# Optimization experiments

Hardware: AMD Instinct MI355X
Metric: run time of the kernel (lower is better)

## Reference

```python
import jax, jax.numpy as jnp
import numpy as np

HEADS = 8
DIM_HEAD = 64
QUERY_DIM = 512
CONTEXT_DIM = 768
INNER = HEADS * DIM_HEAD  # 512
SCALE = DIM_HEAD ** -0.5


def setup_inputs() -> dict:
    key = jax.random.key(0)
    ks = jax.random.split(key, 7)
    B, N, M = 4, 2048, 2048
    x = jax.random.normal(ks[0], (B, N, QUERY_DIM), dtype=jnp.float32)
    context = jax.random.normal(ks[1], (B, M, CONTEXT_DIM), dtype=jnp.float32)
    # torch Linear weights: [out_features, in_features], y = x @ W.T
    s = 0.02
    Wq = jax.random.normal(ks[2], (INNER, QUERY_DIM), dtype=jnp.float32) * s
    Wk = jax.random.normal(ks[3], (INNER, CONTEXT_DIM), dtype=jnp.float32) * s
    Wv = jax.random.normal(ks[4], (INNER, CONTEXT_DIM), dtype=jnp.float32) * s
    Wo = jax.random.normal(ks[5], (QUERY_DIM, INNER), dtype=jnp.float32) * s
    bo = jax.random.normal(ks[6], (QUERY_DIM,), dtype=jnp.float32) * s
    return {"x": x, "context": context, "Wq": Wq, "Wk": Wk, "Wv": Wv, "Wo": Wo, "bo": bo}


def reference(x, context, Wq, Wk, Wv, Wo, bo):
    b, n, _ = x.shape
    m = context.shape[1]
    h, d = HEADS, DIM_HEAD
    # Projections (bias=False for q/k/v)
    q = jnp.einsum('bnc,ec->bne', x, Wq)        # [b, n, inner]
    k = jnp.einsum('bmc,ec->bme', context, Wk)  # [b, m, inner]
    v = jnp.einsum('bmc,ec->bme', context, Wv)
    # Split heads
    q = q.reshape(b, n, h, d)
    k = k.reshape(b, m, h, d)
    v = v.reshape(b, m, h, d)
    # Scores in fp32 (original casts q,k to float), scaled by dim_head**-0.5
    sim = jnp.einsum('bihd,bjhd->bhij', q.astype(jnp.float32), k.astype(jnp.float32)) * SCALE
    attn = jax.nn.softmax(sim, axis=-1).astype(v.dtype)
    out = jnp.einsum('bhij,bjhd->bihd', attn, v).reshape(b, n, h * d)
    # Output projection with bias (dropout=0 -> identity)
    return jnp.einsum('bne,oe->bno', out, Wo) + bo
```

## Files before the change

### kernel.cpp

```cpp
#include <hip/hip_runtime.h>
#include <hip/hip_bf16.h>
#include <math.h>


typedef __bf16 bf16x8 __attribute__((ext_vector_type(8)));
typedef __bf16 bf16x4 __attribute__((ext_vector_type(4)));
typedef short s16x4 __attribute__((ext_vector_type(4)));
typedef float f32x4 __attribute__((ext_vector_type(4)));

#define QSCALE 0.18033688011112042f

#if __has_builtin(__builtin_amdgcn_exp2f)
#define EXP2(x) __builtin_amdgcn_exp2f(x)
#else
#define EXP2(x) exp2f(x)
#endif

__device__ __forceinline__ f32x4 mfma32(bf16x8 a, bf16x8 b, f32x4 c) {
  return __builtin_amdgcn_mfma_f32_16x16x32_bf16(a, b, c, 0, 0, 0);
}
__device__ __forceinline__ f32x4 mfma16(s16x4 a, s16x4 b, f32x4 c) {
  return __builtin_amdgcn_mfma_f32_16x16x16bf16_1k(a, b, c, 0, 0, 0);
}

__device__ __forceinline__ void glds16(const void* g, void* l) {
  __builtin_amdgcn_global_load_lds(
      (const __attribute__((address_space(1))) unsigned int*)g,
      (__attribute__((address_space(3))) unsigned int*)l, 16, 0, 0);
}

__global__ __launch_bounds__(256) void cast_all(
    const float* __restrict__ x, const float* __restrict__ ctx,
    const float* __restrict__ wq, const float* __restrict__ wk,
    const float* __restrict__ wv, const float* __restrict__ wo,
    __bf16* __restrict__ xb, __bf16* __restrict__ cb,
    __bf16* __restrict__ wqb, __bf16* __restrict__ wkb,
    __bf16* __restrict__ wvb, __bf16* __restrict__ wob) {
  const int B0 = 1048576;
  const int B1 = 2621440;
  const int B2 = 2686976;
  const int B3 = 2785280;
  const int B4 = 2883584;
  const int B5 = 2949120;
  for (int i = blockIdx.x * blockDim.x + threadIdx.x; i < B5;
       i += gridDim.x * blockDim.x) {
    const float* s;
    __bf16* d;
    int off;
    if (i < B0)      { s = x;   d = xb;  off = i; }
    else if (i < B1) { s = ctx; d = cb;  off = i - B0; }
    else if (i < B2) { s = wq;  d = wqb; off = i - B1; }
    else if (i < B3) { s = wk;  d = wkb; off = i - B2; }
    else if (i < B4) { s = wv;  d = wvb; off = i - B3; }
    else             { s = wo;  d = wob; off = i - B4; }
    float4 f = ((const float4*)s)[off];
    union { __bf16 b[4]; ushort4 u; } cv;
    cv.b[0] = (__bf16)f.x; cv.b[1] = (__bf16)f.y;
    cv.b[2] = (__bf16)f.z; cv.b[3] = (__bf16)f.w;
    ((ushort4*)d)[off] = cv.u;
  }
}

template <int MODE>
__device__ __forceinline__ void gemm_body(
    const __bf16* __restrict__ A, const __bf16* __restrict__ B,
    __bf16* __restrict__ Cout, int Kd, float scale, int m0, int n0,
    __bf16 (*As)[4][128][8], __bf16 (*Bs)[4][128][8]) {
  const int t = threadIdx.x;
  const int w = t >> 6;
  const int lane = t & 63;
  const int ln = lane & 15;
  const int qd = lane >> 4;
  const int wm = (w >> 1) * 64;
  const int wn = (w & 1) * 64;

  f32x4 zero4 = {0.f, 0.f, 0.f, 0.f};
  f32x4 acc[4][4];
#pragma unroll
  for (int i = 0; i < 4; ++i)
#pragma unroll
    for (int j = 0; j < 4; ++j) acc[i][j] = zero4;

  const __bf16* gA0 = A + (size_t)(m0 + lane) * Kd + w * 8;
  const __bf16* gA1 = A + (size_t)(m0 + 64 + lane) * Kd + w * 8;
  const __bf16* gB0 = B + (size_t)(n0 + lane) * Kd + w * 8;
  const __bf16* gB1 = B + (size_t)(n0 + 64 + lane) * Kd + w * 8;

  glds16(gA0, &As[0][w][0][0]);
  glds16(gA1, &As[0][w][64][0]);
  glds16(gB0, &Bs[0][w][0][0]);
  glds16(gB1, &Bs[0][w][64][0]);

  int buf = 0;
  for (int kc = 0; kc < Kd; kc += 32) {
    __syncthreads();
    if (kc + 32 < Kd) {
      glds16(gA0 + kc + 32, &As[buf ^ 1][w][0][0]);
      glds16(gA1 + kc + 32, &As[buf ^ 1][w][64][0]);
      glds16(gB0 + kc + 32, &Bs[buf ^ 1][w][0][0]);
      glds16(gB1 + kc + 32, &Bs[buf ^ 1][w][64][0]);
    }
    bf16x8 af[4], bfr[4];
#pragma unroll
    for (int i = 0; i < 4; ++i) {
      af[i] = *(const bf16x8*)&As[buf][qd][wm + i * 16 + ln][0];
      bfr[i] = *(const bf16x8*)&Bs[buf][qd][wn + i * 16 + ln][0];
    }
#pragma unroll
    for (int i = 0; i < 4; ++i)
#pragma unroll
      for (int j = 0; j < 4; ++j) {
        if (MODE == 1)
          acc[i][j] = mfma32(af[i], bfr[j], acc[i][j]);
        else
          acc[i][j] = mfma32(bfr[j], af[i], acc[i][j]);
      }
    buf ^= 1;
  }

#pragma unroll
  for (int i = 0; i < 4; ++i)
#pragma unroll
    for (int j = 0; j < 4; ++j) {
      if (MODE == 0) {
        const int gm = m0 + wm + i * 16 + ln;
        const int gn0 = n0 + wn + j * 16 + qd * 4;
        const int bb = gm >> 11, tok = gm & 2047;
        const int hh = gn0 >> 6, dd0 = gn0 & 63;
        bf16x4 v;
#pragma unroll
        for (int rg = 0; rg < 4; ++rg) v[rg] = (__bf16)(acc[i][j][rg] * scale);
        *(bf16x4*)(Cout + (((size_t)bb * 8 + hh) * 2048 + tok) * 64 + dd0) = v;
      } else {
        const int gm0 = m0 + wm + i * 16 + qd * 4;
        const int gn = n0 + wn + j * 16 + ln;
        const int bb = gm0 >> 11, tok0 = gm0 & 2047;
        const int hh = gn >> 6, dd = gn & 63;
        bf16x4 v;
#pragma unroll
        for (int rg = 0; rg < 4; ++rg) v[rg] = (__bf16)acc[i][j][rg];
        *(bf16x4*)(Cout + (((size_t)bb * 8 + hh) * 64 + dd) * 2048 + tok0) = v;
      }
    }
}

__global__ __launch_bounds__(256, 3) void proj_qkv(
    const __bf16* __restrict__ xb, const __bf16* __restrict__ cb,
    const __bf16* __restrict__ Wq, const __bf16* __restrict__ Wk,
    const __bf16* __restrict__ Wv, __bf16* __restrict__ Qw,
    __bf16* __restrict__ Kw, __bf16* __restrict__ Vtw) {
  __shared__ __align__(16) __bf16 As[2][4][128][8];
  __shared__ __align__(16) __bf16 Bs[2][4][128][8];
  const int m0 = blockIdx.x * 128;
  const int job = blockIdx.y >> 2;
  const int n0 = (blockIdx.y & 3) * 128;
  if (job == 0)
    gemm_body<0>(xb, Wq, Qw, 512, QSCALE, m0, n0, As, Bs);
  else if (job == 1)
    gemm_body<0>(cb, Wk, Kw, 768, 1.0f, m0, n0, As, Bs);
  else
    gemm_body<1>(cb, Wv, Vtw, 768, 1.0f, m0, n0, As, Bs);
}

__global__ __launch_bounds__(256) void gemm_out(
    const __bf16* __restrict__ O0, const __bf16* __restrict__ O1,
    const float* __restrict__ lbuf,
    const __bf16* __restrict__ B,
    float* __restrict__ C, const float* __restrict__ bias) {
  const int m0 = blockIdx.x * 64;
  const int n0 = blockIdx.y * 128;
  const int t = threadIdx.x;
  const int w = t >> 6;
  const int lane = t & 63;
  const int ln = lane & 15;
  const int qd = lane >> 4;
  const int wm = (w >> 1) * 32;
  const int wn = (w & 1) * 64;

  __shared__ __align__(16) __bf16 As[2][64][40];
  __shared__ __align__(16) __bf16 Bs[2][4][128][8];

  f32x4 zero4 = {0.f, 0.f, 0.f, 0.f};
  f32x4 acc[2][4];
#pragma unroll
  for (int i = 0; i < 2; ++i)
#pragma unroll
    for (int j = 0; j < 4; ++j) acc[i][j] = zero4;

  const int ra = t >> 2, ca = (t & 3) * 8;
  const int gm_s = m0 + ra;
  const int bidx = gm_s >> 11, tok_s = gm_s & 2047;
  const size_t aoff = (size_t)gm_s * 512 + ca;
  const __bf16* gB0 = B + (size_t)(n0 + lane) * 512 + w * 8;
  const __bf16* gB1 = B + (size_t)(n0 + 64 + lane) * 512 + w * 8;

  float inv[8];
#pragma unroll
  for (int hh = 0; hh < 8; ++hh) {
    const float l0 = lbuf[((size_t)bidx * 8 + hh) * 2048 + tok_s];
    const float l1 = lbuf[65536 + ((size_t)bidx * 8 + hh) * 2048 + tok_s];
    inv[hh] = 1.0f / (l0 + l1);
  }

  {
    union { bf16x8 v; uint4 u; } u0, u1, rr;
    u0.u = *(const uint4*)(O0 + aoff);
    u1.u = *(const uint4*)(O1 + aoff);
    glds16(gB0, &Bs[0][w][0][0]);
    glds16(gB1, &Bs[0][w][64][0]);
    const float iv = inv[0];
#pragma unroll
    for (int e = 0; e < 8; ++e)
      rr.v[e] = (__bf16)(((float)u0.v[e] + (float)u1.v[e]) * iv);
    *(uint4*)&As[0][ra][ca] = rr.u;
  }

  int buf = 0;
#pragma unroll
  for (int k = 0; k < 16; ++k) {
    __syncthreads();
    uint4 o0n, o1n;
    if (k < 15) {
      o0n = *(const uint4*)(O0 + aoff + (k + 1) * 32);
      o1n = *(const uint4*)(O1 + aoff + (k + 1) * 32);
      glds16(gB0 + (k + 1) * 32, &Bs[buf ^ 1][w][0][0]);
      glds16(gB1 + (k + 1) * 32, &Bs[buf ^ 1][w][64][0]);
    }
    bf16x8 af[2], bfr[4];
#pragma unroll
    for (int i = 0; i < 2; ++i)
      af[i] = *(const bf16x8*)&As[buf][wm + i * 16 + ln][qd * 8];
#pragma unroll
    for (int j = 0; j < 4; ++j)
      bfr[j] = *(const bf16x8*)&Bs[buf][qd][wn + j * 16 + ln][0];
#pragma unroll
    for (int i = 0; i < 2; ++i)
#pragma unroll
      for (int j = 0; j < 4; ++j)
        acc[i][j] = mfma32(bfr[j], af[i], acc[i][j]);
    if (k < 15) {
      union { bf16x8 v; uint4 u; } u0, u1, rr;
      u0.u = o0n;
      u1.u = o1n;
      const float iv = inv[(k + 1) >> 1];
#pragma unroll
      for (int e = 0; e < 8; ++e)
        rr.v[e] = (__bf16)(((float)u0.v[e] + (float)u1.v[e]) * iv);
      *(uint4*)&As[buf ^ 1][ra][ca] = rr.u;
    }
    buf ^= 1;
  }

#pragma unroll
  for (int i = 0; i < 2; ++i)
#pragma unroll
    for (int j = 0; j < 4; ++j) {
      const int gm = m0 + wm + i * 16 + ln;
      const int gn0 = n0 + wn + j * 16 + qd * 4;
      f32x4 bi = *(const f32x4*)&bias[gn0];
      f32x4 v = acc[i][j] + bi;
      *(f32x4*)&C[(size_t)gm * 512 + gn0] = v;
    }
}

__global__ __launch_bounds__(256, 4) void attn_kernel(
    const __bf16* __restrict__ Q,
    const __bf16* __restrict__ K,
    const __bf16* __restrict__ Vt,
    __bf16* __restrict__ Oh,
    float* __restrict__ lbuf) {
  const int S = 2048;
  const int qt = blockIdx.x;
  const int bh = blockIdx.y;
  const int sp = blockIdx.z;
  const int b = bh >> 3, h = bh & 7;
  const int t = threadIdx.x;
  const int w = t >> 6;
  const int lane = t & 63;
  const int ln = lane & 15;
  const int qd = lane >> 4;

  __shared__ __align__(16) __bf16 Ks[128][72];
  __shared__ __align__(16) __bf16 Vts[64][132];

  bf16x8 bq[2][2];
  {
    const __bf16* qb =
        Q + ((size_t)bh * S + qt * 128 + w * 32 + ln) * 64 + qd * 8;
#pragma unroll
    for (int mt = 0; mt < 2; ++mt)
#pragma unroll
      for (int kst = 0; kst < 2; ++kst)
        bq[mt][kst] = *(const bf16x8*)(qb + mt * 1024 + kst * 32);
  }

  f32x4 zero4 = {0.f, 0.f, 0.f, 0.f};
  f32x4 o[2][4];
  f32x4 o_l[2];
#pragma unroll
  for (int mt = 0; mt < 2; ++mt) {
#pragma unroll
    for (int i = 0; i < 4; ++i) o[mt][i] = zero4;
    o_l[mt] = zero4;
  }
  const s16x4 ones = {0x3F80, 0x3F80, 0x3F80, 0x3F80};

  const int kr = t >> 1, kc = (t & 1) * 32;
  const int vd = t >> 2, vc = (t & 3) * 32;
  const int kt0 = sp * 8;

  for (int kt = kt0; kt < kt0 + 8; ++kt) {
    const uint4* gK =
        (const uint4*)(K + ((size_t)bh * S + kt * 128 + kr) * 64 + kc);
    const uint4* gV =
        (const uint4*)(Vt + ((size_t)bh * 64 + vd) * S + kt * 128 + vc);
    uint4 kv0 = gK[0], kv1 = gK[1], kv2 = gK[2], kv3 = gK[3];
    uint4 vv0 = gV[0], vv1 = gV[1], vv2 = gV[2], vv3 = gV[3];
    __syncthreads();
    {
      uint4* dK = (uint4*)&Ks[kr][kc];
      dK[0] = kv0; dK[1] = kv1; dK[2] = kv2; dK[3] = kv3;
      uint2* dV = (uint2*)&Vts[vd][vc];
      dV[0] = *(uint2*)&vv0; dV[1] = *((uint2*)&vv0 + 1);
      dV[2] = *(uint2*)&vv1; dV[3] = *((uint2*)&vv1 + 1);
      dV[4] = *(uint2*)&vv2; dV[5] = *((uint2*)&vv2 + 1);
      dV[6] = *(uint2*)&vv3; dV[7] = *((uint2*)&vv3 + 1);
    }
    __syncthreads();

#pragma unroll
    for (int c = 0; c < 4; ++c) {
      f32x4 s[2][2];
      s[0][0] = zero4; s[0][1] = zero4; s[1][0] = zero4; s[1][1] = zero4;
#pragma unroll
      for (int e = 0; e < 2; ++e) {
        const int nt = c * 2 + e;
#pragma unroll
        for (int kst = 0; kst < 2; ++kst) {
          bf16x8 ak = *(const bf16x8*)&Ks[nt * 16 + ln][kst * 32 + qd * 8];
          s[e][0] = mfma32(ak, bq[0][kst], s[e][0]);
          s[e][1] = mfma32(ak, bq[1][kst], s[e][1]);
        }
      }
#pragma unroll
      for (int e = 0; e < 2; ++e)
#pragma unroll
        for (int mt = 0; mt < 2; ++mt)
#pragma unroll
          for (int rg = 0; rg < 4; ++rg) s[e][mt][rg] = EXP2(s[e][mt][rg]);
#pragma unroll
      for (int e = 0; e < 2; ++e) {
        const int nt = c * 2 + e;
        bf16x4 c0, c1;
#pragma unroll
        for (int rg = 0; rg < 4; ++rg) {
          c0[rg] = (__bf16)s[e][0][rg];
          c1[rg] = (__bf16)s[e][1][rg];
        }
        s16x4 p0 = __builtin_bit_cast(s16x4, c0);
        s16x4 p1 = __builtin_bit_cast(s16x4, c1);
        o_l[0] = mfma16(ones, p0, o_l[0]);
        o_l[1] = mfma16(ones, p1, o_l[1]);
#pragma unroll
        for (int i = 0; i < 4; ++i) {
          bf16x4 av = *(const bf16x4*)&Vts[i * 16 + ln][nt * 16 + qd * 4];
          s16x4 a = __builtin_bit_cast(s16x4, av);
          o[0][i] = mfma16(a, p0, o[0][i]);
          o[1][i] = mfma16(a, p1, o[1][i]);
        }
      }
    }
  }

  __bf16* Osp = Oh + (size_t)sp * 8192 * 512;
#pragma unroll
  for (int mt = 0; mt < 2; ++mt) {
    const int tok = qt * 128 + w * 32 + mt * 16 + ln;
    if (qd == 0) lbuf[((size_t)sp * 32 + bh) * 2048 + tok] = o_l[mt][0];
#pragma unroll
    for (int i = 0; i < 4; ++i) {
      bf16x4 v;
#pragma unroll
      for (int rg = 0; rg < 4; ++rg) v[rg] = (__bf16)o[mt][i][rg];
      const int col = h * 64 + i * 16 + qd * 4;
      *(bf16x4*)&Osp[((size_t)b * S + tok) * 512 + col] = v;
    }
  }
}

extern "C" void kernel_launch(void* const* d_in, const int* in_sizes, int n_in,
                              void* d_out, int out_size, void* d_ws,
                              size_t ws_size, hipStream_t stream) {
  const float* x = (const float*)d_in[0];
  const float* ctx = (const float*)d_in[1];
  const float* Wq = (const float*)d_in[2];
  const float* Wk = (const float*)d_in[3];
  const float* Wv = (const float*)d_in[4];
  const float* Wo = (const float*)d_in[5];
  const float* bo = (const float*)d_in[6];

  char* p = (char*)d_ws;
  __bf16* xb = (__bf16*)p;   p += (size_t)8192 * 512 * 2;
  __bf16* cb = (__bf16*)p;   p += (size_t)8192 * 768 * 2;
  __bf16* wqb = (__bf16*)p;  p += (size_t)512 * 512 * 2;
  __bf16* wkb = (__bf16*)p;  p += (size_t)512 * 768 * 2;
  __bf16* wvb = (__bf16*)p;  p += (size_t)512 * 768 * 2;
  __bf16* wob = (__bf16*)p;  p += (size_t)512 * 512 * 2;
  __bf16* Qw = (__bf16*)p;   p += (size_t)8192 * 512 * 2;
  __bf16* Kw = (__bf16*)p;   p += (size_t)8192 * 512 * 2;
  __bf16* Vtw = (__bf16*)p;  p += (size_t)8192 * 512 * 2;
  __bf16* Oh = (__bf16*)p;   p += (size_t)2 * 8192 * 512 * 2;
  float* lbuf = (float*)p;   p += (size_t)2 * 32 * 2048 * 4;

  cast_all<<<2880, 256, 0, stream>>>(x, ctx, Wq, Wk, Wv, Wo, xb, cb, wqb, wkb,
                                     wvb, wob);

  dim3 gp(64, 12);
  proj_qkv<<<gp, 256, 0, stream>>>(xb, cb, wqb, wkb, wvb, Qw, Kw, Vtw);

  dim3 ga(16, 32, 2);
  attn_kernel<<<ga, 256, 0, stream>>>(Qw, Kw, Vtw, Oh, lbuf);

  dim3 go(128, 4);
  gemm_out<<<go, 256, 0, stream>>>(Oh, Oh + (size_t)8192 * 512, lbuf, wob,
                                   (float*)d_out, bo);
}
```

Measured before the change: 204.0 us.

## Use 16x16x32 MFMA for PV and replace async LDS loads with register staging

The attention PV product and row-sum now use the 16x16x32 bf16 MFMA instead of pairs of 16x16x16 ops. K rows are stored in LDS under a permuted row order and V is held in a chunked layout, so each lane's 8-element P fragment lines up with one bf16x8 V read. Both projection GEMMs drop global_load_lds double buffering in favour of register-prefetched 64-wide K tiles in padded single-buffer LDS. The PV change halves the number of MFMA issues for that step. The GEMM change trades async copies and double buffering for register staging, which adds registers and an extra barrier per tile.

```diff
diff --git a/kernel.cpp b/kernel.cpp
--- a/kernel.cpp
+++ b/kernel.cpp
@@ -5,7 +5,6 @@
 
 typedef __bf16 bf16x8 __attribute__((ext_vector_type(8)));
 typedef __bf16 bf16x4 __attribute__((ext_vector_type(4)));
-typedef short s16x4 __attribute__((ext_vector_type(4)));
 typedef float f32x4 __attribute__((ext_vector_type(4)));
 
 #define QSCALE 0.18033688011112042f
@@ -18,15 +17,6 @@
 
 __device__ __forceinline__ f32x4 mfma32(bf16x8 a, bf16x8 b, f32x4 c) {
   return __builtin_amdgcn_mfma_f32_16x16x32_bf16(a, b, c, 0, 0, 0);
-}
-__device__ __forceinline__ f32x4 mfma16(s16x4 a, s16x4 b, f32x4 c) {
-  return __builtin_amdgcn_mfma_f32_16x16x16bf16_1k(a, b, c, 0, 0, 0);
-}
-
-__device__ __forceinline__ void glds16(const void* g, void* l) {
-  __builtin_amdgcn_global_load_lds(
-      (const __attribute__((address_space(1))) unsigned int*)g,
-      (__attribute__((address_space(3))) unsigned int*)l, 16, 0, 0);
 }
 
 __global__ __launch_bounds__(256) void cast_all(
@@ -63,9 +53,9 @@
 
 template <int MODE>
 __device__ __forceinline__ void gemm_body(
-    const __bf16* __restrict__ A, const __bf16* __restrict__ B,
+    const __bf16* __restrict__ A, const __bf16* __restrict__ W,
     __bf16* __restrict__ Cout, int Kd, float scale, int m0, int n0,
-    __bf16 (*As)[4][128][8], __bf16 (*Bs)[4][128][8]) {
+    __bf16 (*As)[72], __bf16 (*Bs)[72]) {
   const int t = threadIdx.x;
   const int w = t >> 6;
   const int lane = t & 63;
@@ -81,41 +71,53 @@
 #pragma unroll
     for (int j = 0; j < 4; ++j) acc[i][j] = zero4;
 
-  const __bf16* gA0 = A + (size_t)(m0 + lane) * Kd + w * 8;
-  const __bf16* gA1 = A + (size_t)(m0 + 64 + lane) * Kd + w * 8;
-  const __bf16* gB0 = B + (size_t)(n0 + lane) * Kd + w * 8;
-  const __bf16* gB1 = B + (size_t)(n0 + 64 + lane) * Kd + w * 8;
-
-  glds16(gA0, &As[0][w][0][0]);
-  glds16(gA1, &As[0][w][64][0]);
-  glds16(gB0, &Bs[0][w][0][0]);
-  glds16(gB1, &Bs[0][w][64][0]);
-
-  int buf = 0;
-  for (int kc = 0; kc < Kd; kc += 32) {
-    __syncthreads();
-    if (kc + 32 < Kd) {
-      glds16(gA0 + kc + 32, &As[buf ^ 1][w][0][0]);
-      glds16(gA1 + kc + 32, &As[buf ^ 1][w][64][0]);
-      glds16(gB0 + kc + 32, &Bs[buf ^ 1][w][0][0]);
-      glds16(gB1 + kc + 32, &Bs[buf ^ 1][w][64][0]);
-    }
-    bf16x8 af[4], bfr[4];
-#pragma unroll
-    for (int i = 0; i < 4; ++i) {
-      af[i] = *(const bf16x8*)&As[buf][qd][wm + i * 16 + ln][0];
-      bfr[i] = *(const bf16x8*)&Bs[buf][qd][wn + i * 16 + ln][0];
-    }
-#pragma unroll
-    for (int i = 0; i < 4; ++i)
-#pragma unroll
-      for (int j = 0; j < 4; ++j) {
-        if (MODE == 1)
-          acc[i][j] = mfma32(af[i], bfr[j], acc[i][j]);
-        else
-          acc[i][j] = mfma32(bfr[j], af[i], acc[i][j]);
+  const int r0 = t >> 2;
+  const int c0 = (t & 3) * 16;
+  const __bf16* gA0 = A + (size_t)(m0 + r0) * Kd + c0;
+  const __bf16* gA1 = A + (size_t)(m0 + r0 + 64) * Kd + c0;
+  const __bf16* gB0 = W + (size_t)(n0 + r0) * Kd + c0;
+  const __bf16* gB1 = W + (size_t)(n0 + r0 + 64) * Kd + c0;
+
+  uint4 a00 = *(const uint4*)gA0, a01 = *(const uint4*)(gA0 + 8);
+  uint4 a10 = *(const uint4*)gA1, a11 = *(const uint4*)(gA1 + 8);
+  uint4 b00 = *(const uint4*)gB0, b01 = *(const uint4*)(gB0 + 8);
+  uint4 b10 = *(const uint4*)gB1, b11 = *(const uint4*)(gB1 + 8);
+
+  for (int kc = 0; kc < Kd; kc += 64) {
+    __syncthreads();
+    *(uint4*)&As[r0][c0] = a00;       *(uint4*)&As[r0][c0 + 8] = a01;
+    *(uint4*)&As[r0 + 64][c0] = a10;  *(uint4*)&As[r0 + 64][c0 + 8] = a11;
+    *(uint4*)&Bs[r0][c0] = b00;       *(uint4*)&Bs[r0][c0 + 8] = b01;
+    *(uint4*)&Bs[r0 + 64][c0] = b10;  *(uint4*)&Bs[r0 + 64][c0 + 8] = b11;
+    __syncthreads();
+    if (kc + 64 < Kd) {
+      a00 = *(const uint4*)(gA0 + kc + 64);
+      a01 = *(const uint4*)(gA0 + kc + 72);
+      a10 = *(const uint4*)(gA1 + kc + 64);
+      a11 = *(const uint4*)(gA1 + kc + 72);
+      b00 = *(const uint4*)(gB0 + kc + 64);
+      b01 = *(const uint4*)(gB0 + kc + 72);
+      b10 = *(const uint4*)(gB1 + kc + 64);
+      b11 = *(const uint4*)(gB1 + kc + 72);
+    }
+#pragma unroll
+    for (int kst = 0; kst < 2; ++kst) {
+      bf16x8 af[4], bfr[4];
+#pragma unroll
+      for (int i = 0; i < 4; ++i) {
+        af[i] = *(const bf16x8*)&As[wm + i * 16 + ln][kst * 32 + qd * 8];
+        bfr[i] = *(const bf16x8*)&Bs[wn + i * 16 + ln][kst * 32 + qd * 8];
       }
-    buf ^= 1;
+#pragma unroll
+      for (int i = 0; i < 4; ++i)
+#pragma unroll
+        for (int j = 0; j < 4; ++j) {
+          if (MODE == 1)
+            acc[i][j] = mfma32(af[i], bfr[j], acc[i][j]);
+          else
+            acc[i][j] = mfma32(bfr[j], af[i], acc[i][j]);
+        }
+    }
   }
 
 #pragma unroll
@@ -149,8 +151,8 @@
     const __bf16* __restrict__ Wq, const __bf16* __restrict__ Wk,
     const __bf16* __restrict__ Wv, __bf16* __restrict__ Qw,
     __bf16* __restrict__ Kw, __bf16* __restrict__ Vtw) {
-  __shared__ __align__(16) __bf16 As[2][4][128][8];
-  __shared__ __align__(16) __bf16 Bs[2][4][128][8];
+  __shared__ __align__(16) __bf16 As[128][72];
+  __shared__ __align__(16) __bf16 Bs[128][72];
   const int m0 = blockIdx.x * 128;
   const int job = blockIdx.y >> 2;
   const int n0 = (blockIdx.y & 3) * 128;
@@ -177,8 +179,8 @@
   const int wm = (w >> 1) * 32;
   const int wn = (w & 1) * 64;
 
-  __shared__ __align__(16) __bf16 As[2][64][40];
-  __shared__ __align__(16) __bf16 Bs[2][4][128][8];
+  __shared__ __align__(16) __bf16 As[64][72];
+  __shared__ __align__(16) __bf16 Bs[128][72];
 
   f32x4 zero4 = {0.f, 0.f, 0.f, 0.f};
   f32x4 acc[2][4];
@@ -187,12 +189,13 @@
 #pragma unroll
     for (int j = 0; j < 4; ++j) acc[i][j] = zero4;
 
-  const int ra = t >> 2, ca = (t & 3) * 8;
-  const int gm_s = m0 + ra;
+  const int r0 = t >> 2;
+  const int c0 = (t & 3) * 16;
+  const int gm_s = m0 + r0;
   const int bidx = gm_s >> 11, tok_s = gm_s & 2047;
-  const size_t aoff = (size_t)gm_s * 512 + ca;
-  const __bf16* gB0 = B + (size_t)(n0 + lane) * 512 + w * 8;
-  const __bf16* gB1 = B + (size_t)(n0 + 64 + lane) * 512 + w * 8;
+  const size_t aoff = (size_t)gm_s * 512 + c0;
+  const __bf16* gB0 = B + (size_t)(n0 + r0) * 512 + c0;
+  const __bf16* gB1 = B + (size_t)(n0 + r0 + 64) * 512 + c0;
 
   float inv[8];
 #pragma unroll
@@ -202,53 +205,53 @@
     inv[hh] = 1.0f / (l0 + l1);
   }
 
-  {
-    union { bf16x8 v; uint4 u; } u0, u1, rr;
-    u0.u = *(const uint4*)(O0 + aoff);
-    u1.u = *(const uint4*)(O1 + aoff);
-    glds16(gB0, &Bs[0][w][0][0]);
-    glds16(gB1, &Bs[0][w][64][0]);
-    const float iv = inv[0];
+  uint4 o00 = *(const uint4*)(O0 + aoff), o01 = *(const uint4*)(O0 + aoff + 8);
+  uint4 o10 = *(const uint4*)(O1 + aoff), o11 = *(const uint4*)(O1 + aoff + 8);
+  uint4 b00 = *(const uint4*)gB0, b01 = *(const uint4*)(gB0 + 8);
+  uint4 b10 = *(const uint4*)gB1, b11 = *(const uint4*)(gB1 + 8);
+
+  for (int kc = 0; kc < 512; kc += 64) {
+    const float iv = inv[kc >> 6];
+    union { bf16x8 v; uint4 u; } u0, u1, r0v, r1v;
+    u0.u = o00; u1.u = o10;
 #pragma unroll
     for (int e = 0; e < 8; ++e)
-      rr.v[e] = (__bf16)(((float)u0.v[e] + (float)u1.v[e]) * iv);
-    *(uint4*)&As[0][ra][ca] = rr.u;
-  }
-
-  int buf = 0;
-#pragma unroll
-  for (int k = 0; k < 16; ++k) {
-    __syncthreads();
-    uint4 o0n, o1n;
-    if (k < 15) {
-      o0n = *(const uint4*)(O0 + aoff + (k + 1) * 32);
-      o1n = *(const uint4*)(O1 + aoff + (k + 1) * 32);
-      glds16(gB0 + (k + 1) * 32, &Bs[buf ^ 1][w][0][0]);
-      glds16(gB1 + (k + 1) * 32, &Bs[buf ^ 1][w][64][0]);
-    }
-    bf16x8 af[2], bfr[4];
-#pragma unroll
-    for (int i = 0; i < 2; ++i)
-      af[i] = *(const bf16x8*)&As[buf][wm + i * 16 + ln][qd * 8];
-#pragma unroll
-    for (int j = 0; j < 4; ++j)
-      bfr[j] = *(const bf16x8*)&Bs[buf][qd][wn + j * 16 + ln][0];
-#pragma unroll
-    for (int i = 0; i < 2; ++i)
+      r0v.v[e] = (__bf16)(((float)u0.v[e] + (float)u1.v[e]) * iv);
+    u0.u = o01; u1.u = o11;
+#pragma unroll
+    for (int e = 0; e < 8; ++e)
+      r1v.v[e] = (__bf16)(((float)u0.v[e] + (float)u1.v[e]) * iv);
+    __syncthreads();
+    *(uint4*)&As[r0][c0] = r0v.u;
+    *(uint4*)&As[r0][c0 + 8] = r1v.u;
+    *(uint4*)&Bs[r0][c0] = b00;       *(uint4*)&Bs[r0][c0 + 8] = b01;
+    *(uint4*)&Bs[r0 + 64][c0] = b10;  *(uint4*)&Bs[r0 + 64][c0 + 8] = b11;
+    __syncthreads();
+    if (kc + 64 < 512) {
+      o00 = *(const uint4*)(O0 + aoff + kc + 64);
+      o01 = *(const uint4*)(O0 + aoff + kc + 72);
+      o10 = *(const uint4*)(O1 + aoff + kc + 64);
+      o11 = *(const uint4*)(O1 + aoff + kc + 72);
+      b00 = *(const uint4*)(gB0 + kc + 64);
+      b01 = *(const uint4*)(gB0 + kc + 72);
+      b10 = *(const uint4*)(gB1 + kc + 64);
+      b11 = *(const uint4*)(gB1 + kc + 72);
+    }
+#pragma unroll
+    for (int kst = 0; kst < 2; ++kst) {
+      bf16x8 af[2], bfr[4];
+#pragma unroll
+      for (int i = 0; i < 2; ++i)
+        af[i] = *(const bf16x8*)&As[wm + i * 16 + ln][kst * 32 + qd * 8];
 #pragma unroll
       for (int j = 0; j < 4; ++j)
-        acc[i][j] = mfma32(bfr[j], af[i], acc[i][j]);
-    if (k < 15) {
-      union { bf16x8 v; uint4 u; } u0, u1, rr;
-      u0.u = o0n;
-      u1.u = o1n;
-      const float iv = inv[(k + 1) >> 1];
-#pragma unroll
-      for (int e = 0; e < 8; ++e)
-        rr.v[e] = (__bf16)(((float)u0.v[e] + (float)u1.v[e]) * iv);
-      *(uint4*)&As[buf ^ 1][ra][ca] = rr.u;
-    }
-    buf ^= 1;
+        bfr[j] = *(const bf16x8*)&Bs[wn + j * 16 + ln][kst * 32 + qd * 8];
+#pragma unroll
+      for (int i = 0; i < 2; ++i)
+#pragma unroll
+        for (int j = 0; j < 4; ++j)
+          acc[i][j] = mfma32(bfr[j], af[i], acc[i][j]);
+    }
   }
 
 #pragma unroll
@@ -281,7 +284,7 @@
   const int qd = lane >> 4;
 
   __shared__ __align__(16) __bf16 Ks[128][72];
-  __shared__ __align__(16) __bf16 Vts[64][132];
+  __shared__ __align__(16) __bf16 V4[4][64][40];
 
   bf16x8 bq[2][2];
   {
@@ -303,28 +306,33 @@
     for (int i = 0; i < 4; ++i) o[mt][i] = zero4;
     o_l[mt] = zero4;
   }
-  const s16x4 ones = {0x3F80, 0x3F80, 0x3F80, 0x3F80};
+  bf16x8 ones8;
+  {
+    union { unsigned short u[8]; bf16x8 v; } U;
+#pragma unroll
+    for (int e = 0; e < 8; ++e) U.u[e] = 0x3F80;
+    ones8 = U.v;
+  }
 
   const int kr = t >> 1, kc = (t & 1) * 32;
-  const int vd = t >> 2, vc = (t & 3) * 32;
+  const int krow =
+      (kr & ~31) | ((kr & 4) << 2) | (((kr >> 3) & 3) << 2) | (kr & 3);
+  const int vd = t >> 2, cV = t & 3;
   const int kt0 = sp * 8;
 
   for (int kt = kt0; kt < kt0 + 8; ++kt) {
     const uint4* gK =
         (const uint4*)(K + ((size_t)bh * S + kt * 128 + kr) * 64 + kc);
     const uint4* gV =
-        (const uint4*)(Vt + ((size_t)bh * 64 + vd) * S + kt * 128 + vc);
+        (const uint4*)(Vt + ((size_t)bh * 64 + vd) * S + kt * 128 + cV * 32);
     uint4 kv0 = gK[0], kv1 = gK[1], kv2 = gK[2], kv3 = gK[3];
     uint4 vv0 = gV[0], vv1 = gV[1], vv2 = gV[2], vv3 = gV[3];
     __syncthreads();
     {
-      uint4* dK = (uint4*)&Ks[kr][kc];
+      uint4* dK = (uint4*)&Ks[krow][kc];
       dK[0] = kv0; dK[1] = kv1; dK[2] = kv2; dK[3] = kv3;
-      uint2* dV = (uint2*)&Vts[vd][vc];
-      dV[0] = *(uint2*)&vv0; dV[1] = *((uint2*)&vv0 + 1);
-      dV[2] = *(uint2*)&vv1; dV[3] = *((uint2*)&vv1 + 1);
-      dV[4] = *(uint2*)&vv2; dV[5] = *((uint2*)&vv2 + 1);
-      dV[6] = *(uint2*)&vv3; dV[7] = *((uint2*)&vv3 + 1);
+      uint4* dV = (uint4*)&V4[cV][vd][0];
+      dV[0] = vv0; dV[1] = vv1; dV[2] = vv2; dV[3] = vv3;
     }
     __syncthreads();
 
@@ -348,26 +356,22 @@
         for (int mt = 0; mt < 2; ++mt)
 #pragma unroll
           for (int rg = 0; rg < 4; ++rg) s[e][mt][rg] = EXP2(s[e][mt][rg]);
-#pragma unroll
-      for (int e = 0; e < 2; ++e) {
-        const int nt = c * 2 + e;
-        bf16x4 c0, c1;
+      bf16x8 p[2];
+#pragma unroll
+      for (int mt = 0; mt < 2; ++mt) {
 #pragma unroll
         for (int rg = 0; rg < 4; ++rg) {
-          c0[rg] = (__bf16)s[e][0][rg];
-          c1[rg] = (__bf16)s[e][1][rg];
+          p[mt][rg] = (__bf16)s[0][mt][rg];
+          p[mt][rg + 4] = (__bf16)s[1][mt][rg];
         }
-        s16x4 p0 = __builtin_bit_cast(s16x4, c0);
-        s16x4 p1 = __builtin_bit_cast(s16x4, c1);
-        o_l[0] = mfma16(ones, p0, o_l[0]);
-        o_l[1] = mfma16(ones, p1, o_l[1]);
-#pragma unroll
-        for (int i = 0; i < 4; ++i) {
-          bf16x4 av = *(const bf16x4*)&Vts[i * 16 + ln][nt * 16 + qd * 4];
-          s16x4 a = __builtin_bit_cast(s16x4, av);
-          o[0][i] = mfma16(a, p0, o[0][i]);
-          o[1][i] = mfma16(a, p1, o[1][i]);
-        }
+      }
+      o_l[0] = mfma32(ones8, p[0], o_l[0]);
+      o_l[1] = mfma32(ones8, p[1], o_l[1]);
+#pragma unroll
+      for (int i = 0; i < 4; ++i) {
+        bf16x8 av = *(const bf16x8*)&V4[c][i * 16 + ln][qd * 8];
+        o[0][i] = mfma32(av, p[0], o[0][i]);
+        o[1][i] = mfma32(av, p[1], o[1][i]);
       }
     }
   }
```

After: 177.5 us. 1.15x faster.
